# Kernel optimization log

Measured on AMD Instinct MI355X. Metric: run time of the kernel, lower is better.

## Reference

```python
import jax, jax.numpy as jnp
import numpy as np

NUM_HEADS = 16


def setup_inputs() -> dict:
    key = jax.random.key(0)
    ks = jax.random.split(key, 5)
    B, S, H = 2, 2048, 1024
    scale = 0.02
    return {
        "x": jax.random.normal(ks[0], (B, S, H), dtype=jnp.float32),
        "w_qkv": jax.random.normal(ks[1], (H, 3 * H), dtype=jnp.float32) * scale,
        "b_qkv": jax.random.normal(ks[2], (3 * H,), dtype=jnp.float32) * scale,
        "w_out": jax.random.normal(ks[3], (H, H), dtype=jnp.float32) * scale,
        "b_out": jax.random.normal(ks[4], (H,), dtype=jnp.float32) * scale,
    }


def reference(x, w_qkv, b_qkv, w_out, b_out):
    B, S, H = x.shape
    nh = NUM_HEADS
    hd = H // nh
    attn_scale = 1.0 / np.sqrt(hd).astype(np.float32)

    qkv = x @ w_qkv + b_qkv                       # (B, S, 3H)
    q, k, v = jnp.split(qkv, 3, axis=-1)
    # (B, S, H) -> (B, nh, S, hd)
    to_heads = lambda t: t.reshape(B, S, nh, hd).transpose(0, 2, 1, 3)
    q, k, v = to_heads(q), to_heads(k), to_heads(v)

    scores = jnp.einsum("bhid,bhjd->bhij", q, k) * attn_scale  # (B, nh, S, S)
    # Source masks where triu(ones)==0 -> strictly-lower triangle masked;
    # allowed positions are j >= i (attends to present and future).
    i = jnp.arange(S)[:, None]
    j = jnp.arange(S)[None, :]
    scores = jnp.where(j >= i, scores, -jnp.inf)
    attn = jax.nn.softmax(scores, axis=-1)        # dropout is identity (eval)

    out = jnp.einsum("bhij,bhjd->bhid", attn, v)  # (B, nh, S, hd)
    out = out.transpose(0, 2, 1, 3).reshape(B, S, H)
    return out @ w_out + b_out
```

## Files before the change

### kernel.cpp

```cpp
#include <hip/hip_runtime.h>
#include <hip/hip_bf16.h>
#include <stdint.h>
#include <stddef.h>

typedef __bf16 bf16_t;
typedef __bf16 bf16x4 __attribute__((ext_vector_type(4)));
typedef __bf16 bf16x8 __attribute__((ext_vector_type(8)));
typedef float f32x4 __attribute__((ext_vector_type(4)));
typedef float f32x16 __attribute__((ext_vector_type(16)));

#define MFMA16(a, b, c) __builtin_amdgcn_mfma_f32_16x16x32_bf16(a, b, c, 0, 0, 0)
#define MFMA32(a, b, c) __builtin_amdgcn_mfma_f32_32x32x16_bf16(a, b, c, 0, 0, 0)

#define GLL16(g, l)                                                      \
    __builtin_amdgcn_global_load_lds(                                    \
        (const __attribute__((address_space(1))) void*)(g),              \
        (__attribute__((address_space(3))) void*)(l), 16, 0, 0)

#define SEQ 2048
#define NHEAD 16
#define HD 64
#define HID 1024
#define QKV_LD 3072
#define VT_LD 2080

__global__ __launch_bounds__(256)
void prep_kernel(const float* __restrict__ x, const float* __restrict__ w_qkv,
                 const float* __restrict__ w_out, bf16_t* __restrict__ xbf,
                 bf16_t* __restrict__ wqkvT, bf16_t* __restrict__ woutT) {
    int L = blockIdx.x;
    int tid = threadIdx.x;
    if (L < 4096) {
        int i = (L * 256 + tid) * 4;
        float4 v = *(const float4*)(x + i);
        bf16x4 o = {(bf16_t)v.x, (bf16_t)v.y, (bf16_t)v.z, (bf16_t)v.w};
        *(bf16x4*)(xbf + i) = o;
        return;
    }
    __shared__ bf16_t tile[32][33];
    const float* W;
    bf16_t* Wt;
    int N, bx, by;
    if (L < 7168) {
        int r = L - 4096;
        W = w_qkv; Wt = wqkvT; N = 3072; bx = r % 96; by = r / 96;
    } else {
        int r = L - 7168;
        W = w_out; Wt = woutT; N = 1024; bx = r % 32; by = r / 32;
    }
    int K = 1024;
    int n0 = bx * 32, k0 = by * 32;
    int tx = tid & 31, ty = tid >> 5;
#pragma unroll
    for (int i = 0; i < 4; i++)
        tile[ty + i * 8][tx] = (bf16_t)W[(size_t)(k0 + ty + i * 8) * N + n0 + tx];
    __syncthreads();
#pragma unroll
    for (int i = 0; i < 4; i++)
        Wt[(size_t)(n0 + ty + i * 8) * K + k0 + tx] = tile[tx][ty + i * 8];
}

#define STAGE8(GB, LB, KOFF)                                                   \
    do {                                                                       \
        GLL16((GB) + (size_t)srow * K + (KOFF) + ssw,                          \
              (LB) + srow * 64 + (scl << 3));                                  \
        GLL16((GB) + (size_t)(srow + 64) * K + (KOFF) + ssw,                   \
              (LB) + (srow + 64) * 64 + (scl << 3));                           \
    } while (0)

#define STAGE_ALL(ASB, BSB, KOFF)                                              \
    do {                                                                       \
        STAGE8(Bb, (BSB), KOFF);                                               \
        STAGE8(Ab, (ASB), KOFF);                                               \
        STAGE8(Bb + (size_t)128 * K, (BSB) + 128 * 64, KOFF);                  \
        STAGE8(Ab + (size_t)128 * K, (ASB) + 128 * 64, KOFF);                  \
    } while (0)

__global__ __launch_bounds__(512, 2)
void gemm_qkv_8ph(const bf16_t* __restrict__ A, const bf16_t* __restrict__ Bt,
                  const float* __restrict__ bias, bf16_t* __restrict__ C,
                  bf16_t* __restrict__ Vt, int M, int N, int K) {
    __shared__ __align__(16) bf16_t As[2][256][64];
    __shared__ __align__(16) bf16_t Bs[2][256][64];

    int nbx = N >> 8;
    int bid = blockIdx.x;
    int swz = (bid & 7) * (gridDim.x >> 3) + (bid >> 3);
    int m0 = (swz / nbx) << 8;
    int n0 = (swz % nbx) << 8;

    int tid = threadIdx.x;
    int lane = tid & 63;
    int wave = tid >> 6;
    int l16 = lane & 15, quad = lane >> 4;
    int wm = (wave >> 2) << 7;
    int wn = (wave & 3) << 6;

    int srow = tid >> 3;
    int scl = tid & 7;
    int ssw = ((scl ^ (srow & 7)) << 3);

    const bf16_t* Ab = A + (size_t)m0 * K;
    const bf16_t* Bb = Bt + (size_t)n0 * K;

    f32x4 acc[8][4] = {};
    bf16x8 a[4][2], b0[2][2], b1[2][2];

    const int NT = K >> 6;

    STAGE_ALL(&As[0][0][0], &Bs[0][0][0], 0);
    STAGE_ALL(&As[1][0][0], &Bs[1][0][0], 64);
    asm volatile("s_waitcnt vmcnt(8)" ::: "memory");
    __builtin_amdgcn_s_barrier();

    for (int t = 0; t < NT; t++) {
        int buf = t & 1;
        const bf16_t* Asb = &As[buf][0][0];
        const bf16_t* Bsb = &Bs[buf][0][0];
        int k2 = (t + 2) << 6;

#pragma unroll
        for (int mt = 0; mt < 4; mt++) {
            int row = wm + mt * 16 + l16;
#pragma unroll
            for (int ks = 0; ks < 2; ks++)
                a[mt][ks] = *(const bf16x8*)(
                    Asb + row * 64 + (((ks * 4 + quad) ^ (row & 7)) << 3));
        }
#pragma unroll
        for (int nt = 0; nt < 2; nt++) {
            int row = wn + nt * 16 + l16;
#pragma unroll
            for (int ks = 0; ks < 2; ks++)
                b0[nt][ks] = *(const bf16x8*)(
                    Bsb + row * 64 + (((ks * 4 + quad) ^ (row & 7)) << 3));
        }
        __builtin_amdgcn_s_barrier();
        asm volatile("s_waitcnt lgkmcnt(0)" ::: "memory");
        __builtin_amdgcn_s_setprio(1);
#pragma unroll
        for (int mt = 0; mt < 4; mt++)
#pragma unroll
            for (int nt = 0; nt < 2; nt++)
#pragma unroll
                for (int ks = 0; ks < 2; ks++)
                    acc[mt][nt] = MFMA16(a[mt][ks], b0[nt][ks], acc[mt][nt]);
        __builtin_amdgcn_s_setprio(0);
        __builtin_amdgcn_s_barrier();

#pragma unroll
        for (int nt = 0; nt < 2; nt++) {
            int row = wn + 32 + nt * 16 + l16;
#pragma unroll
            for (int ks = 0; ks < 2; ks++)
                b1[nt][ks] = *(const bf16x8*)(
                    Bsb + row * 64 + (((ks * 4 + quad) ^ (row & 7)) << 3));
        }
        __builtin_amdgcn_s_barrier();
        asm volatile("s_waitcnt lgkmcnt(0)" ::: "memory");
        __builtin_amdgcn_s_setprio(1);
#pragma unroll
        for (int mt = 0; mt < 4; mt++)
#pragma unroll
            for (int nt = 0; nt < 2; nt++)
#pragma unroll
                for (int ks = 0; ks < 2; ks++)
                    acc[mt][2 + nt] =
                        MFMA16(a[mt][ks], b1[nt][ks], acc[mt][2 + nt]);
        __builtin_amdgcn_s_setprio(0);
        __builtin_amdgcn_s_barrier();

#pragma unroll
        for (int mt = 0; mt < 4; mt++) {
            int row = wm + 64 + mt * 16 + l16;
#pragma unroll
            for (int ks = 0; ks < 2; ks++)
                a[mt][ks] = *(const bf16x8*)(
                    Asb + row * 64 + (((ks * 4 + quad) ^ (row & 7)) << 3));
        }
        __builtin_amdgcn_s_barrier();
        asm volatile("s_waitcnt lgkmcnt(0)" ::: "memory");
        __builtin_amdgcn_s_setprio(1);
#pragma unroll
        for (int mt = 0; mt < 4; mt++)
#pragma unroll
            for (int nt = 0; nt < 2; nt++)
#pragma unroll
                for (int ks = 0; ks < 2; ks++)
                    acc[4 + mt][nt] =
                        MFMA16(a[mt][ks], b0[nt][ks], acc[4 + mt][nt]);
        __builtin_amdgcn_s_setprio(0);
        __builtin_amdgcn_s_barrier();

        if (t + 2 < NT) {
            STAGE_ALL(&As[buf][0][0], &Bs[buf][0][0], k2);
            asm volatile("s_waitcnt vmcnt(8)" ::: "memory");
        } else if (t + 1 < NT) {
            asm volatile("s_waitcnt vmcnt(0)" ::: "memory");
        }
        __builtin_amdgcn_s_setprio(1);
#pragma unroll
        for (int mt = 0; mt < 4; mt++)
#pragma unroll
            for (int nt = 0; nt < 2; nt++)
#pragma unroll
                for (int ks = 0; ks < 2; ks++)
                    acc[4 + mt][2 + nt] =
                        MFMA16(a[mt][ks], b1[nt][ks], acc[4 + mt][2 + nt]);
        __builtin_amdgcn_s_setprio(0);
        __builtin_amdgcn_s_barrier();
    }

    if (n0 < 2048) {
#pragma unroll
        for (int mi = 0; mi < 8; mi++) {
            int row = m0 + wm + (mi >> 2) * 64 + (mi & 3) * 16 + quad * 4;
#pragma unroll
            for (int ni = 0; ni < 4; ni++) {
                int col = n0 + wn + (ni >> 1) * 32 + (ni & 1) * 16 + l16;
                float bv = bias[col];
#pragma unroll
                for (int r = 0; r < 4; r++)
                    C[(size_t)(row + r) * N + col] = (bf16_t)(acc[mi][ni][r] + bv);
            }
        }
    } else {
#pragma unroll
        for (int mi = 0; mi < 8; mi++) {
            int row = m0 + wm + (mi >> 2) * 64 + (mi & 3) * 16 + quad * 4;
            int b = row >> 11, s = row & 2047;
#pragma unroll
            for (int ni = 0; ni < 4; ni++) {
                int col = n0 + wn + (ni >> 1) * 32 + (ni & 1) * 16 + l16;
                float bv = bias[col];
                int cv = col - 2048;
                int bh = b * 16 + (cv >> 6);
                bf16x4 pk;
#pragma unroll
                for (int r = 0; r < 4; r++)
                    pk[r] = (bf16_t)(acc[mi][ni][r] + bv);
                *(bf16x4*)(Vt + ((size_t)bh * HD + (cv & 63)) * VT_LD + s) = pk;
            }
        }
    }
}

template <typename OutT, int TN>
__global__ __launch_bounds__(256)
void gemm_bt_bias(const bf16_t* __restrict__ A, const bf16_t* __restrict__ Bt,
                  const float* __restrict__ bias, OutT* __restrict__ C,
                  int M, int N, int K) {
    constexpr int NT = TN / 32;
    __shared__ __align__(16) bf16_t As[128][32];
    __shared__ __align__(16) bf16_t Bs[TN][32];

    int m0 = blockIdx.y * 128;
    int n0 = blockIdx.x * TN;
    int tid = threadIdx.x;
    int wave = tid >> 6, lane = tid & 63;
    int quad = lane >> 4, l16 = lane & 15;
    int wm = (wave >> 1) * 64, wn = (wave & 1) * (TN / 2);

    f32x4 acc[4][NT] = {};

    const bf16_t* a_base =
        A + (size_t)(m0 + wave * 32 + (lane >> 2)) * K + (lane & 3) * 8;
    const bf16_t* b_base =
        Bt + (size_t)(n0 + wave * (TN / 4) + (lane >> 2)) * K + (lane & 3) * 8;
    bf16_t* as_base = &As[wave * 32][0];
    bf16_t* bs_base = &Bs[wave * (TN / 4)][0];

    for (int k0 = 0; k0 < K; k0 += 32) {
        GLL16(a_base + k0, as_base);
        GLL16(a_base + 16 * K + k0, as_base + 16 * 32);
        GLL16(b_base + k0, bs_base);
        if (TN == 128) GLL16(b_base + 16 * K + k0, bs_base + 16 * 32);
        __syncthreads();

        bf16x8 af[4], bfr[NT];
#pragma unroll
        for (int t = 0; t < 4; t++)
            af[t] = *(const bf16x8*)(&As[wm + t * 16 + l16][quad * 8]);
#pragma unroll
        for (int t = 0; t < NT; t++)
            bfr[t] = *(const bf16x8*)(&Bs[wn + t * 16 + l16][quad * 8]);
#pragma unroll
        for (int mt = 0; mt < 4; mt++)
#pragma unroll
            for (int nt = 0; nt < NT; nt++)
                acc[mt][nt] = MFMA16(af[mt], bfr[nt], acc[mt][nt]);
        __syncthreads();
    }

#pragma unroll
    for (int mt = 0; mt < 4; mt++) {
        int row = m0 + wm + mt * 16 + quad * 4;
#pragma unroll
        for (int nt = 0; nt < NT; nt++) {
            int col = n0 + wn + nt * 16 + l16;
            float bv = bias[col];
#pragma unroll
            for (int r = 0; r < 4; r++)
                C[(size_t)(row + r) * N + col] = (OutT)(acc[mt][nt][r] + bv);
        }
    }
}

__global__ __launch_bounds__(512, 4)
void attn_kernel(const bf16_t* __restrict__ qkv, const bf16_t* __restrict__ Vt,
                 bf16_t* __restrict__ attn_out) {
    int bh = blockIdx.x;
    int tile = (blockIdx.y < 8) ? blockIdx.y : (23 - blockIdx.y);
    int b = bh >> 4, h = bh & 15;

    int tid = threadIdx.x, wave = tid >> 6, lane = tid & 63;
    int l32 = lane & 31, hi = lane >> 5;
    int ih = wave >> 1, jh = wave & 1;

    const bf16_t* q_g = qkv + (size_t)b * SEQ * QKV_LD + (size_t)h * HD;
    const bf16_t* k_g = q_g + HID;
    const bf16_t* vt_g = Vt + (size_t)bh * HD * VT_LD;

    __shared__ __align__(16) bf16_t Ks[64][72];
    __shared__ __align__(16) bf16_t Vs[64][72];
    __shared__ __align__(16) bf16_t Ps[128][68];
    __shared__ float lsumS[8][32];

    const float QS = 0.125f * 1.44269504088896f;
    int i0 = tile * 128;

    bf16x8 qa[4];
    {
        const bf16_t* qrow = q_g + (size_t)(i0 + ih * 32 + l32) * QKV_LD + hi * 8;
#pragma unroll
        for (int ks = 0; ks < 4; ks++) {
            bf16x8 t = *(const bf16x8*)(qrow + ks * 16);
#pragma unroll
            for (int e = 0; e < 8; e++) qa[ks][e] = (bf16_t)((float)t[e] * QS);
        }
    }

    f32x16 o = {};
    float lsum = 0.0f;

    int sr = tid >> 3, sc = (tid & 7) * 8;

    bf16x8 kr = *(const bf16x8*)(k_g + (size_t)(i0 + sr) * QKV_LD + sc);
    bf16x8 vr = *(const bf16x8*)(vt_g + (size_t)sr * VT_LD + i0 + sc);

    for (int j0 = i0; j0 < SEQ; j0 += 64) {
        __syncthreads();
        *(bf16x8*)(&Ks[sr][sc]) = kr;
        *(bf16x8*)(&Vs[sr][sc]) = vr;
        __syncthreads();

        if (j0 + 64 < SEQ) {
            kr = *(const bf16x8*)(k_g + (size_t)(j0 + 64 + sr) * QKV_LD + sc);
            vr = *(const bf16x8*)(vt_g + (size_t)sr * VT_LD + j0 + 64 + sc);
        }

        f32x16 st = {};
#pragma unroll
        for (int ks = 0; ks < 4; ks++) {
            bf16x8 ka = *(const bf16x8*)(&Ks[jh * 32 + l32][ks * 16 + hi * 8]);
            st = MFMA32(ka, qa[ks], st);
        }

        if (j0 < i0 + 128) {
            int gi = i0 + ih * 32 + l32;
#pragma unroll
            for (int rq = 0; rq < 4; rq++) {
                bf16x4 pk;
#pragma unroll
                for (int r = 0; r < 4; r++) {
                    int gj = j0 + jh * 32 + 8 * rq + 4 * hi + r;
                    float p = (gj >= gi) ? __builtin_amdgcn_exp2f(st[rq * 4 + r]) : 0.0f;
                    lsum += p;
                    pk[r] = (bf16_t)p;
                }
                *(bf16x4*)(&Ps[ih * 32 + l32][jh * 32 + 8 * rq + 4 * hi]) = pk;
            }
        } else {
#pragma unroll
            for (int rq = 0; rq < 4; rq++) {
                bf16x4 pk;
#pragma unroll
                for (int r = 0; r < 4; r++) {
                    float p = __builtin_amdgcn_exp2f(st[rq * 4 + r]);
                    lsum += p;
                    pk[r] = (bf16_t)p;
                }
                *(bf16x4*)(&Ps[ih * 32 + l32][jh * 32 + 8 * rq + 4 * hi]) = pk;
            }
        }
        __syncthreads();

#pragma unroll
        for (int ks = 0; ks < 4; ks++) {
            bf16x8 pa = *(const bf16x8*)(&Ps[ih * 32 + l32][ks * 16 + hi * 8]);
            bf16x8 vb = *(const bf16x8*)(&Vs[jh * 32 + l32][ks * 16 + hi * 8]);
            o = MFMA32(pa, vb, o);
        }
    }

    lsum += __shfl_xor(lsum, 32, 64);
    lsumS[wave][l32] = lsum;
    __syncthreads();

#pragma unroll
    for (int rq = 0; rq < 4; rq++) {
#pragma unroll
        for (int r = 0; r < 4; r++) {
            int il = 8 * rq + 4 * hi + r;
            float rs = lsumS[ih * 2][il] + lsumS[ih * 2 + 1][il];
            int gi = i0 + ih * 32 + il;
            attn_out[(size_t)(b * SEQ + gi) * HID + h * HD + jh * 32 + l32] =
                (bf16_t)(o[rq * 4 + r] / rs);
        }
    }
}

extern "C" void kernel_launch(void* const* d_in, const int* in_sizes, int n_in,
                              void* d_out, int out_size, void* d_ws, size_t ws_size,
                              hipStream_t stream) {
    const float* x     = (const float*)d_in[0];
    const float* w_qkv = (const float*)d_in[1];
    const float* b_qkv = (const float*)d_in[2];
    const float* w_out = (const float*)d_in[3];
    const float* b_out = (const float*)d_in[4];
    float* out = (float*)d_out;

    char* ws = (char*)d_ws;
    bf16_t* xbf   = (bf16_t*)(ws);
    bf16_t* wqkvT = (bf16_t*)(ws + 8388608);
    bf16_t* woutT = (bf16_t*)(ws + 14680064);
    bf16_t* qkv   = (bf16_t*)(ws + 16777216);
    bf16_t* attn  = (bf16_t*)(ws + 41943040);
    bf16_t* Vt    = (bf16_t*)(ws + 50331648);

    prep_kernel<<<8192, 256, 0, stream>>>(x, w_qkv, w_out, xbf, wqkvT, woutT);

    gemm_qkv_8ph<<<192, 512, 0, stream>>>(xbf, wqkvT, b_qkv, qkv, Vt,
                                          4096, 3072, 1024);

    attn_kernel<<<dim3(2 * NHEAD, SEQ / 128), 512, 0, stream>>>(qkv, Vt, attn);

    gemm_bt_bias<float, 64><<<dim3(1024 / 64, 4096 / 128), 256, 0, stream>>>(
        attn, woutT, b_out, out, 4096, 1024, 1024);
}
```

Measured before the change: 178.3 us.

## Keep P in registers via lane shuffles and split PV over key halves

The attention kernel no longer writes the probability tile to shared memory and syncs before the PV MFMA. Each wave instead builds the PV A-operand from its own score registers, exchanging halves across lanes with shuffles. Each wave computes a partial output over its 32-key half for both head-dim halves, and the two partials are reduced through shared memory at the end. This removes one block barrier and the P store/load per key tile, at the cost of twice the output accumulators and an extra final reduction. The output projection GEMM tile width is also raised from 64 to 128.

New measurement: 209.5 us. +17.5%, slower.

```diff
diff --git a/kernel.cpp b/kernel.cpp
--- a/kernel.cpp
+++ b/kernel.cpp
@@ -323,7 +323,7 @@
 
     __shared__ __align__(16) bf16_t Ks[64][72];
     __shared__ __align__(16) bf16_t Vs[64][72];
-    __shared__ __align__(16) bf16_t Ps[128][68];
+    __shared__ float Op[4][32][64];
     __shared__ float lsumS[8][32];
 
     const float QS = 0.125f * 1.44269504088896f;
@@ -340,7 +340,7 @@
         }
     }
 
-    f32x16 o = {};
+    f32x16 o2[2] = {};
     float lsum = 0.0f;
 
     int sr = tid >> 3, sc = (tid & 7) * 8;
@@ -366,56 +366,79 @@
             st = MFMA32(ka, qa[ks], st);
         }
 
+        bf16x4 pk[4];
         if (j0 < i0 + 128) {
             int gi = i0 + ih * 32 + l32;
 #pragma unroll
             for (int rq = 0; rq < 4; rq++) {
-                bf16x4 pk;
 #pragma unroll
                 for (int r = 0; r < 4; r++) {
                     int gj = j0 + jh * 32 + 8 * rq + 4 * hi + r;
                     float p = (gj >= gi) ? __builtin_amdgcn_exp2f(st[rq * 4 + r]) : 0.0f;
                     lsum += p;
-                    pk[r] = (bf16_t)p;
+                    pk[rq][r] = (bf16_t)p;
                 }
-                *(bf16x4*)(&Ps[ih * 32 + l32][jh * 32 + 8 * rq + 4 * hi]) = pk;
             }
         } else {
 #pragma unroll
             for (int rq = 0; rq < 4; rq++) {
-                bf16x4 pk;
 #pragma unroll
                 for (int r = 0; r < 4; r++) {
                     float p = __builtin_amdgcn_exp2f(st[rq * 4 + r]);
                     lsum += p;
-                    pk[r] = (bf16_t)p;
+                    pk[rq][r] = (bf16_t)p;
                 }
-                *(bf16x4*)(&Ps[ih * 32 + l32][jh * 32 + 8 * rq + 4 * hi]) = pk;
-            }
-        }
-        __syncthreads();
-
-#pragma unroll
-        for (int ks = 0; ks < 4; ks++) {
-            bf16x8 pa = *(const bf16x8*)(&Ps[ih * 32 + l32][ks * 16 + hi * 8]);
-            bf16x8 vb = *(const bf16x8*)(&Vs[jh * 32 + l32][ks * 16 + hi * 8]);
-            o = MFMA32(pa, vb, o);
+            }
+        }
+
+#pragma unroll
+        for (int ks2 = 0; ks2 < 2; ks2++) {
+            uint2 snd = *(uint2*)&pk[2 * ks2 + (hi ^ 1)];
+            uint2 own = *(uint2*)&pk[2 * ks2 + hi];
+            uint2 rcv;
+            rcv.x = (unsigned)__shfl_xor((int)snd.x, 32, 64);
+            rcv.y = (unsigned)__shfl_xor((int)snd.y, 32, 64);
+            uint4 fr;
+            if (hi == 0) { fr.x = own.x; fr.y = own.y; fr.z = rcv.x; fr.w = rcv.y; }
+            else         { fr.x = rcv.x; fr.y = rcv.y; fr.z = own.x; fr.w = own.y; }
+            bf16x8 pa = *(bf16x8*)&fr;
+#pragma unroll
+            for (int dt = 0; dt < 2; dt++) {
+                bf16x8 vb = *(const bf16x8*)(
+                    &Vs[dt * 32 + l32][jh * 32 + ks2 * 16 + hi * 8]);
+                o2[dt] = MFMA32(pa, vb, o2[dt]);
+            }
         }
     }
 
     lsum += __shfl_xor(lsum, 32, 64);
     lsumS[wave][l32] = lsum;
+    if (jh == 1) {
+#pragma unroll
+        for (int dt = 0; dt < 2; dt++)
+#pragma unroll
+            for (int rq = 0; rq < 4; rq++)
+#pragma unroll
+                for (int r = 0; r < 4; r++)
+                    Op[ih][8 * rq + 4 * hi + r][dt * 32 + l32] = o2[dt][rq * 4 + r];
+    }
     __syncthreads();
 
-#pragma unroll
-    for (int rq = 0; rq < 4; rq++) {
-#pragma unroll
-        for (int r = 0; r < 4; r++) {
-            int il = 8 * rq + 4 * hi + r;
-            float rs = lsumS[ih * 2][il] + lsumS[ih * 2 + 1][il];
-            int gi = i0 + ih * 32 + il;
-            attn_out[(size_t)(b * SEQ + gi) * HID + h * HD + jh * 32 + l32] =
-                (bf16_t)(o[rq * 4 + r] / rs);
+    if (jh == 0) {
+#pragma unroll
+        for (int rq = 0; rq < 4; rq++) {
+#pragma unroll
+            for (int r = 0; r < 4; r++) {
+                int il = 8 * rq + 4 * hi + r;
+                float rs = lsumS[ih * 2][il] + lsumS[ih * 2 + 1][il];
+                int gi = i0 + ih * 32 + il;
+#pragma unroll
+                for (int dt = 0; dt < 2; dt++) {
+                    float val = o2[dt][rq * 4 + r] + Op[ih][il][dt * 32 + l32];
+                    attn_out[(size_t)(b * SEQ + gi) * HID + h * HD + dt * 32 + l32] =
+                        (bf16_t)(val / rs);
+                }
+            }
         }
     }
 }
@@ -445,6 +468,6 @@
 
     attn_kernel<<<dim3(2 * NHEAD, SEQ / 128), 512, 0, stream>>>(qkv, Vt, attn);
 
-    gemm_bt_bias<float, 64><<<dim3(1024 / 64, 4096 / 128), 256, 0, stream>>>(
+    gemm_bt_bias<float, 128><<<dim3(1024 / 128, 4096 / 128), 256, 0, stream>>>(
         attn, woutT, b_out, out, 4096, 1024, 1024);
 }
```
